# Optimization experiments

Hardware: AMD Instinct MI355X
Metric: run time of the kernel (lower is better)

## Reference

```python
import jax, jax.numpy as jnp
import numpy as np

D = 768
H = 12
HD = D // H
FF = 3072
EPS = 1e-5


def layernorm(x, g, b):
    mu = jnp.mean(x, axis=-1, keepdims=True)
    var = jnp.mean(jnp.square(x - mu), axis=-1, keepdims=True)
    return (x - mu) * jax.lax.rsqrt(var + EPS) * g + b


def setup_inputs() -> dict:
    key = jax.random.key(0)
    ks = jax.random.split(key, 12)
    s = 0.02
    return {
        "x": jax.random.normal(ks[0], (4, 1024, D), dtype=jnp.float32),
        "w_qkv": jax.random.normal(ks[1], (D, 3 * D), dtype=jnp.float32) * s,
        "b_qkv": jnp.zeros((3 * D,), jnp.float32),
        "w_proj": jax.random.normal(ks[2], (D, D), dtype=jnp.float32) * s,
        "b_proj": jnp.zeros((D,), jnp.float32),
        "w1": jax.random.normal(ks[3], (D, FF), dtype=jnp.float32) * s,
        "b1": jnp.zeros((FF,), jnp.float32),
        "w2": jax.random.normal(ks[4], (FF, D), dtype=jnp.float32) * s,
        "b2": jnp.zeros((D,), jnp.float32),
        "g1": jnp.ones((D,), jnp.float32),
        "be1": jnp.zeros((D,), jnp.float32),
        "g2": jnp.ones((D,), jnp.float32),
        "be2": jnp.zeros((D,), jnp.float32),
    }


def reference(x, w_qkv, b_qkv, w_proj, b_proj, w1, b1, w2, b2, g1, be1, g2, be2):
    B, N, C = x.shape
    # --- attention (pre-norm) ---
    h = layernorm(x, g1, be1)
    qkv = (h @ w_qkv + b_qkv).reshape(B, N, 3, H, HD)
    q = jnp.transpose(qkv[:, :, 0], (0, 2, 1, 3))  # [B,H,N,hd]
    k = jnp.transpose(qkv[:, :, 1], (0, 2, 1, 3))
    v = jnp.transpose(qkv[:, :, 2], (0, 2, 1, 3))
    attn = jnp.einsum("bhqd,bhkd->bhqk", q, k) * (HD ** -0.5)
    attn = jax.nn.softmax(attn, axis=-1)
    o = jnp.einsum("bhqk,bhkd->bhqd", attn, v)
    o = jnp.transpose(o, (0, 2, 1, 3)).reshape(B, N, C)
    x = x + (o @ w_proj + b_proj)
    # --- feedforward (pre-norm) ---
    h2 = layernorm(x, g2, be2)
    ff = jax.nn.gelu(h2 @ w1 + b1, approximate=False) @ w2 + b2
    return x + ff
```

## Files before the change

### kernel.cpp

```cpp
#include <hip/hip_runtime.h>
#include <hip/hip_bf16.h>
#include <math.h>

typedef __attribute__((ext_vector_type(8))) short short8;
typedef __attribute__((ext_vector_type(4))) float f32x4;

#define DMODEL 768
#define THREE_D 2304
#define FFDIM 3072
#define NSEQ 1024
#define NHEAD 12
#define HEADD 64
#define MROWS 4096

__device__ __forceinline__ ushort f2bf(float f) {
  union { float f; unsigned u; } c; c.f = f;
  unsigned u = c.u;
  unsigned r = (u + 0x7fffu + ((u >> 16) & 1u)) >> 16;
  return (ushort)r;
}

__device__ __forceinline__ unsigned pack2bf(float a, float b) {
  union { __hip_bfloat162 h; unsigned u; } c;
  c.h = __float22bfloat162_rn(make_float2(a, b));
  return c.u;
}

__device__ __forceinline__ void load_lds16(const ushort* g, const ushort* l) {
  __builtin_amdgcn_global_load_lds(
      (const __attribute__((address_space(1))) unsigned int*)g,
      (__attribute__((address_space(3))) unsigned int*)l, 16, 0, 0);
}

template <int N> __device__ __forceinline__ void wait_vm() {
  if constexpr (N == 8)      asm volatile("s_waitcnt vmcnt(8)" ::: "memory");
  else if constexpr (N == 6) asm volatile("s_waitcnt vmcnt(6)" ::: "memory");
  else if constexpr (N == 4) asm volatile("s_waitcnt vmcnt(4)" ::: "memory");
  else                       asm volatile("s_waitcnt vmcnt(0)" ::: "memory");
}

__global__ __launch_bounds__(256) void ln_kernel(const float* __restrict__ x,
    const float* __restrict__ g, const float* __restrict__ be,
    ushort* __restrict__ out) {
  int row = blockIdx.x;
  const float* xr = x + (size_t)row * DMODEL;
  int tid = threadIdx.x;
  float v0 = xr[tid], v1 = xr[tid + 256], v2 = xr[tid + 512];
  __shared__ float red1[4], red2[4];
  float s = v0 + v1 + v2;
  #pragma unroll
  for (int off = 32; off; off >>= 1) s += __shfl_xor(s, off);
  if ((tid & 63) == 0) red1[tid >> 6] = s;
  __syncthreads();
  float mean = (red1[0] + red1[1] + red1[2] + red1[3]) * (1.0f / 768.0f);
  float d0 = v0 - mean, d1 = v1 - mean, d2 = v2 - mean;
  float q = d0 * d0 + d1 * d1 + d2 * d2;
  #pragma unroll
  for (int off = 32; off; off >>= 1) q += __shfl_xor(q, off);
  if ((tid & 63) == 0) red2[tid >> 6] = q;
  __syncthreads();
  float var = (red2[0] + red2[1] + red2[2] + red2[3]) * (1.0f / 768.0f);
  float rs = rsqrtf(var + 1e-5f);
  size_t base = (size_t)row * DMODEL;
  out[base + tid]       = f2bf(d0 * rs * g[tid]       + be[tid]);
  out[base + tid + 256] = f2bf(d1 * rs * g[tid + 256] + be[tid + 256]);
  out[base + tid + 512] = f2bf(d2 * rs * g[tid + 512] + be[tid + 512]);
}

__global__ void wt_kernel(const float* __restrict__ W, ushort* __restrict__ Wt,
                          int K, int N) {
  __shared__ float t[32][33];
  int n0 = blockIdx.x * 32, k0 = blockIdx.y * 32;
  int tx = threadIdx.x, ty = threadIdx.y;
  #pragma unroll
  for (int r = 0; r < 4; r++)
    t[ty + r * 8][tx] = W[(size_t)(k0 + ty + r * 8) * N + n0 + tx];
  __syncthreads();
  #pragma unroll
  for (int r = 0; r < 4; r++)
    Wt[(size_t)(n0 + ty + r * 8) * K + k0 + tx] = f2bf(t[tx][ty + r * 8]);
}

__global__ void vt_kernel(const ushort* __restrict__ qkv, ushort* __restrict__ Vt) {
  __shared__ ushort t[32][33];
  int n0 = blockIdx.x * 32, d0 = blockIdx.y * 32, bh = blockIdx.z;
  int b = bh / NHEAD, hh = bh % NHEAD;
  int tx = threadIdx.x, ty = threadIdx.y;
  #pragma unroll
  for (int r = 0; r < 4; r++)
    t[ty + r * 8][tx] = qkv[(size_t)(b * NSEQ + n0 + ty + r * 8) * THREE_D +
                            2 * DMODEL + hh * HEADD + d0 + tx];
  __syncthreads();
  #pragma unroll
  for (int r = 0; r < 4; r++) {
    int n = n0 + tx;
    int np = (n & ~63) | (((n & 15) << 2) | ((n >> 4) & 3));
    Vt[((size_t)bh * HEADD + d0 + ty + r * 8) * NSEQ + np] = t[tx][ty + r * 8];
  }
}

template <int BN, int MODE>
__global__ __launch_bounds__(512, 2) void gemm256_kernel(
    const ushort* __restrict__ A, const ushort* __restrict__ Bt,
    const float* __restrict__ bias, void* __restrict__ Cout,
    int gx, int Ntot, int K) {
  constexpr int FN = BN / 64;
  constexpr int WN = BN / 4;
  constexpr int ABUF = (256 + BN) * 64;
  constexpr int BOFF = 256 * 64;
  __shared__ ushort S[2 * ABUF];
  int tid = threadIdx.x, lane = tid & 63, wave = tid >> 6;
  int wm = wave >> 2, wn = wave & 3;
  int rsel = lane & 15, quad = lane >> 4;
  int nwg = gridDim.x;
  int o = blockIdx.x;
  int wg = (o & 7) * (nwg >> 3) + (o >> 3);
  int bx = wg % gx, by = wg / gx;
  int m0 = by * 256, n0 = bx * BN;
  f32x4 acc[8][FN] = {};
  int xorc = (rsel & 7) * 8;

  auto SA = [&](int buf, int k0, int i) {
    int c0 = i * 512 + wave * 64;
    int c = c0 + lane, r = c >> 3;
    int kk = ((c ^ r) & 7) * 8;
    load_lds16(&A[(size_t)(m0 + r) * K + k0 + kk], S + buf * ABUF + c0 * 8);
  };
  auto SB = [&](int buf, int k0, int i) {
    int c0 = i * 512 + wave * 64;
    int c = c0 + lane, r = c >> 3;
    int kk = ((c ^ r) & 7) * 8;
    load_lds16(&Bt[(size_t)(n0 + r) * K + k0 + kk],
               S + buf * ABUF + BOFF + c0 * 8);
  };

  #pragma unroll
  for (int i = 0; i < 4; i++) SA(0, 0, i);
  #pragma unroll
  for (int i = 0; i < FN; i++) SB(0, 0, i);
  wait_vm<0>();
  __builtin_amdgcn_s_barrier();

  int ntk = K >> 6;
  for (int t = 0; t < ntk; t++) {
    int cur = t & 1, nxt = cur ^ 1;
    bool pre = (t + 1 < ntk);
    int nk0 = (t + 1) * 64;
    short8 bfr[FN];
    #pragma unroll
    for (int p = 0; p < 4; p++) {
      const int ks = p >> 1, half = p & 1;
      const int ko = ks * 32 + quad * 8;
      short8 af[4];
      #pragma unroll
      for (int mi = 0; mi < 4; mi++) {
        int R = wm * 128 + (half * 4 + mi) * 16 + rsel;
        af[mi] = *(const short8*)&S[cur * ABUF + R * 64 + (ko ^ xorc)];
      }
      if (half == 0) {
        #pragma unroll
        for (int ni = 0; ni < FN; ni++) {
          int R = wn * WN + ni * 16 + rsel;
          bfr[ni] = *(const short8*)&S[cur * ABUF + BOFF + R * 64 + (ko ^ xorc)];
        }
      }
      if (pre) {
        if (p == 0) {
          #pragma unroll
          for (int i = 0; i < FN; i++) SB(nxt, nk0, i);
          SA(nxt, nk0, 0);
        } else if (p == 1) {
          SA(nxt, nk0, 1); SA(nxt, nk0, 2); SA(nxt, nk0, 3);
        }
      }
      __builtin_amdgcn_s_barrier();
      asm volatile("s_waitcnt lgkmcnt(0)" ::: "memory");
      __builtin_amdgcn_sched_barrier(0);
      __builtin_amdgcn_s_setprio(1);
      #pragma unroll
      for (int mi = 0; mi < 4; mi++)
        #pragma unroll
        for (int ni = 0; ni < FN; ni++)
          acc[half * 4 + mi][ni] = __builtin_amdgcn_mfma_f32_16x16x32_bf16(
              af[mi], bfr[ni], acc[half * 4 + mi][ni], 0, 0, 0);
      __builtin_amdgcn_s_setprio(0);
    }
    wait_vm<0>();
    __builtin_amdgcn_s_barrier();
  }
  ushort* Cl = S;
  float bv[FN];
  #pragma unroll
  for (int ni = 0; ni < FN; ni++) bv[ni] = bias[n0 + wn * WN + ni * 16 + rsel];
  #pragma unroll
  for (int mi = 0; mi < 8; mi++) {
    int row = wm * 128 + mi * 16 + quad * 4;
    #pragma unroll
    for (int ni = 0; ni < FN; ni++) {
      int col = wn * WN + ni * 16 + rsel;
      #pragma unroll
      for (int j = 0; j < 4; j++) {
        float v = acc[mi][ni][j] + bv[ni];
        if (MODE == 2) v = 0.5f * v * (1.0f + erff(v * 0.70710678118654752f));
        Cl[(row + j) * 200 + col] = f2bf(v);
      }
    }
  }
  __syncthreads();
  constexpr int CPR = BN / 8;
  ushort* Cg = (ushort*)Cout;
  for (int c = tid; c < 256 * CPR; c += 512) {
    int row = c / CPR, off = c - row * CPR;
    int4 v = *(const int4*)&Cl[row * 200 + off * 8];
    *(int4*)&Cg[(size_t)(m0 + row) * Ntot + n0 + off * 8] = v;
  }
}

template <int BM, int BN>
__global__ __launch_bounds__(256) void gemm_kernel(
    const ushort* __restrict__ A, const ushort* __restrict__ Bt,
    const float* __restrict__ bias, const float* __restrict__ resid,
    float* __restrict__ Cout, int gx, int Ntot, int K) {
  constexpr int ABUF = (BM + BN) * 64;
  constexpr int BOFF = BM * 64;
  __shared__ ushort S[2 * ABUF];
  constexpr int WM = BM / 2, WN = BN / 2;
  constexpr int FM = WM / 16, FN = WN / 16;
  constexpr int NL = BM / 32 + BN / 32;
  int tid = threadIdx.x, lane = tid & 63, wave = tid >> 6;
  int wm = wave >> 1, wn = wave & 1;
  int rsel = lane & 15, quad = lane >> 4;
  int nwg = gridDim.x;
  int o = blockIdx.x;
  int wg = (o & 7) * (nwg >> 3) + (o >> 3);
  int bx = wg % gx, by = wg / gx;
  int m0 = by * BM, n0 = bx * BN;
  f32x4 acc[FM][FN] = {};

  auto STAGE = [&](int buf, int k0) {
    #pragma unroll
    for (int i = 0; i < BM / 32; i++) {
      int c0 = i * 256 + wave * 64;
      int c = c0 + lane, r = c >> 3;
      int kk = ((c ^ r) & 7) * 8;
      load_lds16(&A[(size_t)(m0 + r) * K + k0 + kk], S + buf * ABUF + c0 * 8);
    }
    #pragma unroll
    for (int i = 0; i < BN / 32; i++) {
      int c0 = i * 256 + wave * 64;
      int c = c0 + lane, r = c >> 3;
      int kk = ((c ^ r) & 7) * 8;
      load_lds16(&Bt[(size_t)(n0 + r) * K + k0 + kk],
                 S + buf * ABUF + BOFF + c0 * 8);
    }
  };

  STAGE(0, 0);
  int ntk = K >> 6;
  for (int t = 0; t < ntk; t++) {
    int cur = t & 1;
    if (t + 1 < ntk) {
      STAGE(cur ^ 1, (t + 1) * 64);
      wait_vm<NL>();
    } else {
      wait_vm<0>();
    }
    __builtin_amdgcn_s_barrier();
    #pragma unroll
    for (int ks = 0; ks < 2; ks++) {
      short8 af[FM], bfr[FN];
      int ko = ks * 32 + quad * 8;
      #pragma unroll
      for (int mi = 0; mi < FM; mi++) {
        int R = wm * WM + mi * 16 + rsel;
        af[mi] = *(const short8*)&S[cur * ABUF + R * 64 + (ko ^ ((R & 7) * 8))];
      }
      #pragma unroll
      for (int ni = 0; ni < FN; ni++) {
        int R = wn * WN + ni * 16 + rsel;
        bfr[ni] = *(const short8*)&S[cur * ABUF + BOFF + R * 64 + (ko ^ ((R & 7) * 8))];
      }
      #pragma unroll
      for (int mi = 0; mi < FM; mi++)
        #pragma unroll
        for (int ni = 0; ni < FN; ni++)
          acc[mi][ni] = __builtin_amdgcn_mfma_f32_16x16x32_bf16(
              af[mi], bfr[ni], acc[mi][ni], 0, 0, 0);
    }
    asm volatile("s_waitcnt lgkmcnt(0)" ::: "memory");
    __builtin_amdgcn_s_barrier();
  }
  float* Cl = (float*)S;
  #pragma unroll
  for (int ni = 0; ni < FN; ni++) {
    int col = wn * WN + ni * 16 + rsel;
    float bvv = bias[n0 + col];
    #pragma unroll
    for (int mi = 0; mi < FM; mi++) {
      int row = wm * WM + mi * 16 + quad * 4;
      #pragma unroll
      for (int j = 0; j < 4; j++)
        Cl[(row + j) * 68 + col] = acc[mi][ni][j] + bvv;
    }
  }
  __syncthreads();
  constexpr int CPR = BN / 4;
  for (int c = tid; c < BM * CPR; c += 256) {
    int row = c / CPR, off = c - row * CPR;
    size_t gi = (size_t)(m0 + row) * Ntot + n0 + off * 4;
    float4 v = *(const float4*)&Cl[row * 68 + off * 4];
    float4 rr = *(const float4*)&resid[gi];
    v.x += rr.x; v.y += rr.y; v.z += rr.z; v.w += rr.w;
    *(float4*)&Cout[gi] = v;
  }
}

__global__ __launch_bounds__(256) void attn_kernel(
    const ushort* __restrict__ qkv, const ushort* __restrict__ Vt,
    ushort* __restrict__ o) {
  __shared__ ushort Klds[2][64][64];
  __shared__ ushort Vlds[2][64][64];
  __shared__ ushort Plds[4][16][72];
  const float CL2 = 0.18033688011112042f;
  int tid = threadIdx.x, lane = tid & 63, wave = tid >> 6;
  int qt = blockIdx.x, bh = blockIdx.y;
  int b = bh / NHEAD, hh = bh % NHEAD;
  int q0 = qt * 64;
  int rsel = lane & 15, quad = lane >> 4;
  int xorc = (rsel & 7) * 8;

  short8 qf[2];
  {
    int qrow = q0 + wave * 16 + rsel;
    const ushort* qp = qkv + (size_t)(b * NSEQ + qrow) * THREE_D + hh * HEADD + quad * 8;
    qf[0] = *(const short8*)qp;
    qf[1] = *(const short8*)(qp + 32);
  }
  short8 onesf;
  #pragma unroll
  for (int i = 0; i < 8; i++) onesf[i] = (short)0x3F80;

  int r0 = tid >> 3, d0 = (tid & 7) * 8;
  int c1 = tid + 256, r1 = c1 >> 3, d1 = (c1 & 7) * 8;
  int sw0 = d0 ^ ((r0 & 7) * 8), sw1 = d1 ^ ((r1 & 7) * 8);
  const ushort* Kg = qkv + (size_t)b * NSEQ * THREE_D + DMODEL + hh * HEADD;
  const ushort* Vg = Vt + (size_t)bh * HEADD * NSEQ;
  int4 kr0, kr1, vr0, vr1;
  auto LD = [&](int kv0) {
    kr0 = *(const int4*)&Kg[(size_t)(kv0 + r0) * THREE_D + d0];
    kr1 = *(const int4*)&Kg[(size_t)(kv0 + r1) * THREE_D + d1];
    vr0 = *(const int4*)&Vg[(size_t)r0 * NSEQ + kv0 + d0];
    vr1 = *(const int4*)&Vg[(size_t)r1 * NSEQ + kv0 + d1];
  };
  auto ST = [&](int bf) {
    *(int4*)&Klds[bf][r0][sw0] = kr0;
    *(int4*)&Klds[bf][r1][sw1] = kr1;
    *(int4*)&Vlds[bf][r0][sw0] = vr0;
    *(int4*)&Vlds[bf][r1][sw1] = vr1;
  };

  f32x4 oacc[4] = {};
  f32x4 osum = {};

  LD(0); ST(0); __syncthreads();

  for (int t = 0; t < 16; t++) {
    int bf = t & 1;
    if (t < 15) LD((t + 1) * 64);
    f32x4 sfr[4] = {};
    __builtin_amdgcn_s_setprio(1);
    #pragma unroll
    for (int ks = 0; ks < 2; ks++) {
      int ko = ks * 32 + quad * 8;
      #pragma unroll
      for (int nt = 0; nt < 4; nt++) {
        short8 kf = *(const short8*)&Klds[bf][nt * 16 + rsel][ko ^ xorc];
        sfr[nt] = __builtin_amdgcn_mfma_f32_16x16x32_bf16(qf[ks], kf, sfr[nt], 0, 0, 0);
      }
    }
    __builtin_amdgcn_s_setprio(0);
    #pragma unroll
    for (int i = 0; i < 4; i++) {
      float p0 = exp2f(fmaf(sfr[0][i], CL2, -12.0f));
      float p1 = exp2f(fmaf(sfr[1][i], CL2, -12.0f));
      float p2 = exp2f(fmaf(sfr[2][i], CL2, -12.0f));
      float p3 = exp2f(fmaf(sfr[3][i], CL2, -12.0f));
      uint2 pw = make_uint2(pack2bf(p0, p1), pack2bf(p2, p3));
      *(uint2*)&Plds[wave][quad * 4 + i][rsel * 4] = pw;
    }
    __builtin_amdgcn_s_setprio(1);
    #pragma unroll
    for (int ks = 0; ks < 2; ks++) {
      int ko = ks * 32 + quad * 8;
      short8 pf = *(const short8*)&Plds[wave][rsel][ko];
      #pragma unroll
      for (int nt = 0; nt < 4; nt++) {
        short8 vf = *(const short8*)&Vlds[bf][nt * 16 + rsel][ko ^ xorc];
        oacc[nt] = __builtin_amdgcn_mfma_f32_16x16x32_bf16(pf, vf, oacc[nt], 0, 0, 0);
      }
      osum = __builtin_amdgcn_mfma_f32_16x16x32_bf16(pf, onesf, osum, 0, 0, 0);
    }
    __builtin_amdgcn_s_setprio(0);
    if (t < 15) ST(bf ^ 1);
    __syncthreads();
  }
  float rin[4];
  #pragma unroll
  for (int i = 0; i < 4; i++) rin[i] = __builtin_amdgcn_rcpf(osum[i]);
  #pragma unroll
  for (int nt = 0; nt < 4; nt++)
    #pragma unroll
    for (int i = 0; i < 4; i++) {
      int qrow = q0 + wave * 16 + quad * 4 + i;
      int col = hh * HEADD + nt * 16 + rsel;
      o[(size_t)(b * NSEQ + qrow) * DMODEL + col] = f2bf(oacc[nt][i] * rin[i]);
    }
}

extern "C" void kernel_launch(void* const* d_in, const int* in_sizes, int n_in,
                              void* d_out, int out_size, void* d_ws, size_t ws_size,
                              hipStream_t stream) {
  const float* x      = (const float*)d_in[0];
  const float* w_qkv  = (const float*)d_in[1];
  const float* b_qkv  = (const float*)d_in[2];
  const float* w_proj = (const float*)d_in[3];
  const float* b_proj = (const float*)d_in[4];
  const float* w1     = (const float*)d_in[5];
  const float* b1     = (const float*)d_in[6];
  const float* w2     = (const float*)d_in[7];
  const float* b2     = (const float*)d_in[8];
  const float* g1     = (const float*)d_in[9];
  const float* be1    = (const float*)d_in[10];
  const float* g2     = (const float*)d_in[11];
  const float* be2    = (const float*)d_in[12];
  float* out = (float*)d_out;

  char* ws = (char*)d_ws;
  ushort* Wqkv_t  = (ushort*)(ws + 0);
  ushort* Wproj_t = (ushort*)(ws + 3538944);
  ushort* W1_t    = (ushort*)(ws + 4718592);
  ushort* W2_t    = (ushort*)(ws + 9437184);
  ushort* hbuf    = (ushort*)(ws + 14155776);
  ushort* qkv     = (ushort*)(ws + 20447232);
  ushort* ff1     = qkv;
  ushort* VtB     = (ushort*)(ws + 45613056);
  ushort* obuf    = (ushort*)(ws + 51904512);
  float*  x2      = (float*)(ws + 58195968);

  dim3 tb(32, 8);
  wt_kernel<<<dim3(THREE_D / 32, DMODEL / 32), tb, 0, stream>>>(w_qkv, Wqkv_t, DMODEL, THREE_D);
  wt_kernel<<<dim3(DMODEL / 32, DMODEL / 32), tb, 0, stream>>>(w_proj, Wproj_t, DMODEL, DMODEL);
  wt_kernel<<<dim3(FFDIM / 32, DMODEL / 32), tb, 0, stream>>>(w1, W1_t, DMODEL, FFDIM);
  wt_kernel<<<dim3(DMODEL / 32, FFDIM / 32), tb, 0, stream>>>(w2, W2_t, FFDIM, DMODEL);

  ln_kernel<<<MROWS, 256, 0, stream>>>(x, g1, be1, hbuf);

  gemm256_kernel<192, 0><<<192, 512, 0, stream>>>(
      hbuf, Wqkv_t, b_qkv, qkv, THREE_D / 192, THREE_D, DMODEL);

  vt_kernel<<<dim3(NSEQ / 32, HEADD / 32, 4 * NHEAD), tb, 0, stream>>>(qkv, VtB);

  attn_kernel<<<dim3(NSEQ / 64, 4 * NHEAD), 256, 0, stream>>>(qkv, VtB, obuf);

  gemm_kernel<128, 64><<<384, 256, 0, stream>>>(
      obuf, Wproj_t, b_proj, x, x2, DMODEL / 64, DMODEL, DMODEL);

  ln_kernel<<<MROWS, 256, 0, stream>>>(x2, g2, be2, hbuf);

  gemm256_kernel<192, 2><<<256, 512, 0, stream>>>(
      hbuf, W1_t, b1, ff1, FFDIM / 192, FFDIM, DMODEL);

  gemm_kernel<128, 64><<<384, 256, 0, stream>>>(
      ff1, W2_t, b2, x2, out, DMODEL / 64, DMODEL, FFDIM);

  (void)in_sizes; (void)n_in; (void)out_size; (void)ws_size;
}
```

Baseline: 162.2 us.

## Merge weight transposes into one launch and double-buffer LDS fragment reads in GEMMs

The four weight-transpose launches are combined into one kernel that picks the matrix from a flat block index, which removes three launches. In the 256-row GEMM, A/B fragments for the next MFMA phase are now read from LDS before the current MFMAs run, and the per-phase lgkmcnt wait and sched_barrier are dropped, so LDS latency can overlap with MFMA work. The smaller GEMM loads both k-step fragments before issuing any MFMAs. Together these add register pressure and depend on the compiler inserting correct waits now that the explicit ones are gone.

Measured after the change: 156.3 us. -3.6%, faster.

```diff
diff --git a/kernel.cpp b/kernel.cpp
--- a/kernel.cpp
+++ b/kernel.cpp
@@ -67,10 +67,19 @@
   out[base + tid + 512] = f2bf(d2 * rs * g[tid + 512] + be[tid + 512]);
 }
 
-__global__ void wt_kernel(const float* __restrict__ W, ushort* __restrict__ Wt,
-                          int K, int N) {
+__global__ void wt_all_kernel(
+    const float* __restrict__ w_qkv, const float* __restrict__ w_proj,
+    const float* __restrict__ w1, const float* __restrict__ w2,
+    ushort* __restrict__ Wqkv_t, ushort* __restrict__ Wproj_t,
+    ushort* __restrict__ W1_t, ushort* __restrict__ W2_t) {
   __shared__ float t[32][33];
-  int n0 = blockIdx.x * 32, k0 = blockIdx.y * 32;
+  int id = blockIdx.x;
+  const float* W; ushort* Wt; int K, N, bx, by;
+  if (id < 1728)      { W = w_qkv;  Wt = Wqkv_t;  K = 768;  N = 2304; bx = id % 72; by = id / 72; }
+  else if (id < 2304) { id -= 1728; W = w_proj; Wt = Wproj_t; K = 768;  N = 768;  bx = id % 24; by = id / 24; }
+  else if (id < 4608) { id -= 2304; W = w1;     Wt = W1_t;    K = 768;  N = 3072; bx = id % 96; by = id / 96; }
+  else                { id -= 4608; W = w2;     Wt = W2_t;    K = 3072; N = 768;  bx = id % 24; by = id / 24; }
+  int n0 = bx * 32, k0 = by * 32;
   int tx = threadIdx.x, ty = threadIdx.y;
   #pragma unroll
   for (int r = 0; r < 4; r++)
@@ -133,6 +142,15 @@
     load_lds16(&Bt[(size_t)(n0 + r) * K + k0 + kk],
                S + buf * ABUF + BOFF + c0 * 8);
   };
+  auto RDA = [&](int cur, int half, int ks, int mi) -> short8 {
+    int R = wm * 128 + (half * 4 + mi) * 16 + rsel;
+    return *(const short8*)&S[cur * ABUF + R * 64 + ((ks * 32 + quad * 8) ^ xorc)];
+  };
+  auto RDB = [&](int cur, int ks, int ni) -> short8 {
+    int R = wn * WN + ni * 16 + rsel;
+    return *(const short8*)&S[cur * ABUF + BOFF + R * 64 +
+                              ((ks * 32 + quad * 8) ^ xorc)];
+  };
 
   #pragma unroll
   for (int i = 0; i < 4; i++) SA(0, 0, i);
@@ -146,22 +164,22 @@
     int cur = t & 1, nxt = cur ^ 1;
     bool pre = (t + 1 < ntk);
     int nk0 = (t + 1) * 64;
-    short8 bfr[FN];
+    short8 afb[2][4], bfb[2][FN];
+    #pragma unroll
+    for (int mi = 0; mi < 4; mi++) afb[0][mi] = RDA(cur, 0, 0, mi);
+    #pragma unroll
+    for (int ni = 0; ni < FN; ni++) bfb[0][ni] = RDB(cur, 0, ni);
     #pragma unroll
     for (int p = 0; p < 4; p++) {
       const int ks = p >> 1, half = p & 1;
-      const int ko = ks * 32 + quad * 8;
-      short8 af[4];
-      #pragma unroll
-      for (int mi = 0; mi < 4; mi++) {
-        int R = wm * 128 + (half * 4 + mi) * 16 + rsel;
-        af[mi] = *(const short8*)&S[cur * ABUF + R * 64 + (ko ^ xorc)];
-      }
-      if (half == 0) {
+      if (p < 3) {
+        const int ksn = (p + 1) >> 1, halfn = (p + 1) & 1;
         #pragma unroll
-        for (int ni = 0; ni < FN; ni++) {
-          int R = wn * WN + ni * 16 + rsel;
-          bfr[ni] = *(const short8*)&S[cur * ABUF + BOFF + R * 64 + (ko ^ xorc)];
+        for (int mi = 0; mi < 4; mi++)
+          afb[(p + 1) & 1][mi] = RDA(cur, halfn, ksn, mi);
+        if (p == 1) {
+          #pragma unroll
+          for (int ni = 0; ni < FN; ni++) bfb[1][ni] = RDB(cur, 1, ni);
         }
       }
       if (pre) {
@@ -173,17 +191,15 @@
           SA(nxt, nk0, 1); SA(nxt, nk0, 2); SA(nxt, nk0, 3);
         }
       }
-      __builtin_amdgcn_s_barrier();
-      asm volatile("s_waitcnt lgkmcnt(0)" ::: "memory");
-      __builtin_amdgcn_sched_barrier(0);
       __builtin_amdgcn_s_setprio(1);
       #pragma unroll
       for (int mi = 0; mi < 4; mi++)
         #pragma unroll
         for (int ni = 0; ni < FN; ni++)
           acc[half * 4 + mi][ni] = __builtin_amdgcn_mfma_f32_16x16x32_bf16(
-              af[mi], bfr[ni], acc[half * 4 + mi][ni], 0, 0, 0);
+              afb[p & 1][mi], bfb[ks][ni], acc[half * 4 + mi][ni], 0, 0, 0);
       __builtin_amdgcn_s_setprio(0);
+      __builtin_amdgcn_s_barrier();
     }
     wait_vm<0>();
     __builtin_amdgcn_s_barrier();
@@ -266,27 +282,29 @@
       wait_vm<0>();
     }
     __builtin_amdgcn_s_barrier();
+    short8 af[2][FM], bf[2][FN];
     #pragma unroll
     for (int ks = 0; ks < 2; ks++) {
-      short8 af[FM], bfr[FN];
       int ko = ks * 32 + quad * 8;
       #pragma unroll
       for (int mi = 0; mi < FM; mi++) {
         int R = wm * WM + mi * 16 + rsel;
-        af[mi] = *(const short8*)&S[cur * ABUF + R * 64 + (ko ^ ((R & 7) * 8))];
+        af[ks][mi] = *(const short8*)&S[cur * ABUF + R * 64 + (ko ^ ((R & 7) * 8))];
       }
       #pragma unroll
       for (int ni = 0; ni < FN; ni++) {
         int R = wn * WN + ni * 16 + rsel;
-        bfr[ni] = *(const short8*)&S[cur * ABUF + BOFF + R * 64 + (ko ^ ((R & 7) * 8))];
-      }
+        bf[ks][ni] = *(const short8*)&S[cur * ABUF + BOFF + R * 64 + (ko ^ ((R & 7) * 8))];
+      }
+    }
+    #pragma unroll
+    for (int ks = 0; ks < 2; ks++)
       #pragma unroll
       for (int mi = 0; mi < FM; mi++)
         #pragma unroll
         for (int ni = 0; ni < FN; ni++)
           acc[mi][ni] = __builtin_amdgcn_mfma_f32_16x16x32_bf16(
-              af[mi], bfr[ni], acc[mi][ni], 0, 0, 0);
-    }
+              af[ks][mi], bf[ks][ni], acc[mi][ni], 0, 0, 0);
     asm volatile("s_waitcnt lgkmcnt(0)" ::: "memory");
     __builtin_amdgcn_s_barrier();
   }
@@ -448,10 +466,8 @@
   float*  x2      = (float*)(ws + 58195968);
 
   dim3 tb(32, 8);
-  wt_kernel<<<dim3(THREE_D / 32, DMODEL / 32), tb, 0, stream>>>(w_qkv, Wqkv_t, DMODEL, THREE_D);
-  wt_kernel<<<dim3(DMODEL / 32, DMODEL / 32), tb, 0, stream>>>(w_proj, Wproj_t, DMODEL, DMODEL);
-  wt_kernel<<<dim3(FFDIM / 32, DMODEL / 32), tb, 0, stream>>>(w1, W1_t, DMODEL, FFDIM);
-  wt_kernel<<<dim3(DMODEL / 32, FFDIM / 32), tb, 0, stream>>>(w2, W2_t, FFDIM, DMODEL);
+  wt_all_kernel<<<6912, tb, 0, stream>>>(w_qkv, w_proj, w1, w2,
+                                         Wqkv_t, Wproj_t, W1_t, W2_t);
 
   ln_kernel<<<MROWS, 256, 0, stream>>>(x, g1, be1, hbuf);
 
```
